# Kernel tuning notes

Measured on AMD Instinct MI355X. Metric: run time of the kernel, lower is better.

## Reference

```python
import jax, jax.numpy as jnp
import numpy as np

EPS = 1e-5


def _conv1x1(x, w, b):
    # x: (B,C,H,W), w: (O,C), b: (O,)
    return jnp.einsum('oc,bchw->bohw', w, x) + b[None, :, None, None]


def _attn(q, k, v):
    # q,k: (B,Dq,H,W); v: (B,C,H,W). Full NxN attention, softmax over keys.
    B, _, H, W = q.shape
    N = H * W
    Q = q.reshape(B, -1, N)
    K = k.reshape(B, -1, N)
    V = v.reshape(B, -1, N)
    A = jax.nn.softmax(jnp.einsum('bci,bcj->bij', Q, K), axis=-1)  # (B,N,N)
    out = jnp.einsum('bcj,bij->bci', V, A)  # out[b,c,i] = sum_j V[b,c,j] A[b,i,j]
    return out.reshape(B, -1, H, W)


def _std(feat):
    # torch.var(dim=2) is unbiased (ddof=1)
    B, C = feat.shape[:2]
    v = jnp.var(feat.reshape(B, C, -1), axis=2, ddof=1) + EPS
    return jnp.sqrt(v)[:, :, None, None]


def _fmm(fb_feat, bg_feat):
    return fb_feat * (_std(bg_feat) / _std(fb_feat))


def setup_inputs() -> dict:
    key = jax.random.key(0)
    ks = jax.random.split(key, 16)
    B, C, H, W = 2, 256, 64, 64
    D = C // 8
    s = 0.05
    inp = {
        'x': jax.random.normal(ks[0], (B, C, H, W), jnp.float32),
        'mask': jax.random.randint(ks[1], (B, 1, H, W), 0, 2).astype(jnp.float32),
        'sa_wq': jax.random.normal(ks[2], (D, C), jnp.float32) * s,
        'sa_bq': jax.random.normal(ks[3], (D,), jnp.float32) * s,
        'sa_wk': jax.random.normal(ks[4], (D, C), jnp.float32) * s,
        'sa_bk': jax.random.normal(ks[5], (D,), jnp.float32) * s,
        'sa_wv': jax.random.normal(ks[6], (C, C), jnp.float32) * s,
        'sa_bv': jax.random.normal(ks[7], (C,), jnp.float32) * s,
        'sa_gamma': jax.random.uniform(ks[8], (1,), jnp.float32),
        'wq': jax.random.normal(ks[9], (D, C), jnp.float32) * s,
        'bq': jax.random.normal(ks[10], (D,), jnp.float32) * s,
        'wk': jax.random.normal(ks[11], (D, C), jnp.float32) * s,
        'bk': jax.random.normal(ks[12], (D,), jnp.float32) * s,
        'wv': jax.random.normal(ks[13], (C, C), jnp.float32) * s,
        'bv': jax.random.normal(ks[14], (C,), jnp.float32) * s,
        'gamma': jax.random.uniform(ks[15], (1,), jnp.float32),
    }
    return inp


def reference(x, mask, sa_wq, sa_bq, sa_wk, sa_bk, sa_wv, sa_bv, sa_gamma,
              wq, bq, wk, bk, wv, bv, gamma):
    # --- Self_Attn ---
    sa_out = _attn(_conv1x1(x, sa_wq, sa_bq),
                   _conv1x1(x, sa_wk, sa_bk),
                   _conv1x1(x, sa_wv, sa_bv))
    x = sa_gamma[0] * sa_out + x
    # --- FB_FMM masked cross attention (mask already at feature resolution) ---
    reverse_mask = 1.0 - mask
    feature_b = reverse_mask * x
    feature_f = mask * x
    sw_bg = _attn(_conv1x1(feature_f, wq, bq),
                  _conv1x1(feature_b, wk, bk),
                  _conv1x1(feature_b, wv, bv))
    out = x + gamma[0] * _fmm(feature_f, sw_bg)
    return out
```

## Files before the change

kernel.cpp:

```cpp
#include <hip/hip_runtime.h>
#include <stdint.h>

typedef _Float16 f16;
typedef __attribute__((ext_vector_type(8))) _Float16 half8;
typedef __attribute__((ext_vector_type(2))) __fp16 fp16x2;
typedef __attribute__((ext_vector_type(8))) short short8;
typedef __attribute__((ext_vector_type(4))) float f32x4;

#define NPOS 4096
#define CCH  256
#define OQK  64
#define BATCH 2
#define NSPLIT 4
#define KEYS_PER_SPLIT 1024

typedef __attribute__((address_space(3))) uint32_t lds_u32;
typedef __attribute__((address_space(1))) const uint32_t glb_u32;

__device__ __forceinline__ float bf2f(short u) {
    union { uint32_t i; float f; } c;
    c.i = ((uint32_t)(uint16_t)u) << 16;
    return c.f;
}
__device__ __forceinline__ short f2bf(float f) {
    union { float f; uint32_t i; } c; c.f = f;
    uint32_t lsb = (c.i >> 16) & 1u;
    c.i += 0x7FFFu + lsb;
    return (short)(c.i >> 16);
}

__device__ __forceinline__ bool detect_bf16(const uint32_t* mw) {
    int hits = 0;
    #pragma unroll
    for (int i = 0; i < 64; ++i) hits += ((mw[i] & 0xFFFFu) == 0x3F80u) ? 1 : 0;
    return hits != 0;
}

__device__ __forceinline__ void load8(const void* base, size_t e0, bool bf, float* v) {
    if (bf) {
        short8 s = *(const short8*)((const short*)base + e0);
        #pragma unroll
        for (int j = 0; j < 8; ++j) v[j] = bf2f(s[j]);
    } else {
        const float* fp = (const float*)base + e0;
        float4 a = *(const float4*)fp;
        float4 b = *(const float4*)(fp + 4);
        v[0] = a.x; v[1] = a.y; v[2] = a.z; v[3] = a.w;
        v[4] = b.x; v[5] = b.y; v[6] = b.z; v[7] = b.w;
    }
}
__device__ __forceinline__ float load1(const void* base, int i, bool bf) {
    return bf ? bf2f(((const short*)base)[i]) : ((const float*)base)[i];
}

__device__ __forceinline__ int pkrtz(float a, float b) {
    union { fp16x2 h; int i; } u;
    u.h = __builtin_amdgcn_cvt_pkrtz(a, b);
    return u.i;
}

__global__ __launch_bounds__(256) void convert_inputs(
    const uint32_t* __restrict__ mask_raw,
    const void* __restrict__ w1q, const void* __restrict__ w1k, const void* __restrict__ w1v_,
    const void* __restrict__ b1q, const void* __restrict__ b1k, const void* __restrict__ b1v_,
    const void* __restrict__ g1,
    const void* __restrict__ w2q, const void* __restrict__ w2k, const void* __restrict__ w2v_,
    const void* __restrict__ b2q, const void* __restrict__ b2k, const void* __restrict__ b2v_,
    const void* __restrict__ g2,
    float* __restrict__ maskf,
    f16* __restrict__ w1qk, f16* __restrict__ w1vm, f16* __restrict__ b1,
    f16* __restrict__ w2qk, f16* __restrict__ w2vm, f16* __restrict__ b2,
    float* __restrict__ gam)
{
    const bool bf = detect_bf16(mask_raw);
    const int blk = blockIdx.x, tid = threadIdx.x;
    float v[8];
    if (blk < 4) {
        const size_t e0 = ((size_t)blk * 256 + tid) * 8;
        load8(mask_raw, e0, bf, v);
        float4 f0 = {v[0], v[1], v[2], v[3]}, f1 = {v[4], v[5], v[6], v[7]};
        *(float4*)(maskf + e0) = f0;
        *(float4*)(maskf + e0 + 4) = f1;
    } else if (blk < 12) {
        const size_t g = ((size_t)(blk - 4) * 256 + tid) * 8;
        const int o = (int)(g >> 8), cc = (int)(g & 255);
        const void* src = (o < 32) ? w1q : w1k;
        const size_t se = (size_t)((o < 32) ? o : o - 32) * 256 + cc;
        load8(src, se, bf, v);
        half8 h;
        #pragma unroll
        for (int j = 0; j < 8; ++j) h[j] = (f16)v[j];
        *(half8*)(w1qk + g) = h;
    } else if (blk < 44) {
        const size_t g = ((size_t)(blk - 12) * 256 + tid) * 8;
        load8(w1v_, g, bf, v);
        half8 h;
        #pragma unroll
        for (int j = 0; j < 8; ++j) h[j] = (f16)v[j];
        *(half8*)(w1vm + g) = h;
    } else if (blk < 52) {
        const size_t g = ((size_t)(blk - 44) * 256 + tid) * 8;
        const int o = (int)(g >> 8), cc = (int)(g & 255);
        const void* src = (o < 32) ? w2q : w2k;
        const size_t se = (size_t)((o < 32) ? o : o - 32) * 256 + cc;
        load8(src, se, bf, v);
        half8 h;
        #pragma unroll
        for (int j = 0; j < 8; ++j) h[j] = (f16)v[j];
        *(half8*)(w2qk + g) = h;
    } else if (blk < 84) {
        const size_t g = ((size_t)(blk - 52) * 256 + tid) * 8;
        load8(w2v_, g, bf, v);
        half8 h;
        #pragma unroll
        for (int j = 0; j < 8; ++j) h[j] = (f16)v[j];
        *(half8*)(w2vm + g) = h;
    } else {
        for (int i = tid; i < 320; i += 256) {
            const void* s1 = (i < 32) ? b1q : (i < 64) ? b1k : b1v_;
            const void* s2 = (i < 32) ? b2q : (i < 64) ? b2k : b2v_;
            const int ii = (i < 32) ? i : (i < 64) ? i - 32 : i - 64;
            b1[i] = (f16)load1(s1, ii, bf);
            b2[i] = (f16)load1(s2, ii, bf);
        }
        if (tid == 0) {
            gam[0] = load1(g1, 0, bf);
            gam[1] = load1(g2, 0, bf);
        }
    }
}

__global__ __launch_bounds__(256) void conv_qkv(
    const void* __restrict__ xin, int is_raw,
    const uint32_t* __restrict__ mask_raw,
    const f16* __restrict__ wqk,
    const f16* __restrict__ wvm,
    const f16* __restrict__ bias,
    const float* __restrict__ maskf, int use_mask,
    f16* __restrict__ qkout,
    f16* __restrict__ vout)
{
    const bool bf = is_raw ? detect_bf16(mask_raw) : false;
    const int b    = blockIdx.y;
    const int n0   = blockIdx.x * 32;
    const int tid  = threadIdx.x;
    const int lane = tid & 63;
    const int w    = tid >> 6;
    const int lo   = lane & 15;
    const int hi   = lane >> 4;

    __shared__ f16 xt[32 * 256];

    {
        const int nc = tid & 3;
        const int cg = tid >> 2;
        #pragma unroll
        for (int it = 0; it < 4; ++it) {
            const int c = cg + 64 * it;
            const size_t off = ((size_t)b * CCH + c) * NPOS + n0 + nc * 8;
            float v8[8];
            load8(xin, off, bf, v8);
            #pragma unroll
            for (int j = 0; j < 8; ++j) {
                const int n = nc * 8 + j;
                int byte = n * 512 + c * 2;
                byte ^= ((n & 7) << 4);
                *(f16*)((char*)xt + byte) = (f16)v8[j];
            }
        }
    }
    __syncthreads();

    const f32x4 z = {0.f, 0.f, 0.f, 0.f};
    f32x4 acc_qk[2];
    f32x4 acc_v[4][2];
    #pragma unroll
    for (int i = 0; i < 2; ++i) {
        acc_qk[i] = z;
        #pragma unroll
        for (int j = 0; j < 4; ++j) acc_v[j][i] = z;
    }

    #pragma unroll 1
    for (int ks = 0; ks < 8; ++ks) {
        const int ce = ks * 32 + 8 * hi;
        half8 xfr[2];
        #pragma unroll
        for (int nt = 0; nt < 2; ++nt) {
            const int n = nt * 16 + lo;
            int byte = n * 512 + ce * 2;
            byte ^= ((n & 7) << 4);
            xfr[nt] = *(const half8*)((const char*)xt + byte);
        }
        {
            half8 wf = *(const half8*)(wqk + (size_t)(w * 16 + lo) * 256 + ce);
            #pragma unroll
            for (int nt = 0; nt < 2; ++nt)
                acc_qk[nt] = __builtin_amdgcn_mfma_f32_16x16x32_f16(xfr[nt], wf, acc_qk[nt], 0, 0, 0);
        }
        #pragma unroll
        for (int ot = 0; ot < 4; ++ot) {
            half8 wf = *(const half8*)(wvm + (size_t)(w * 64 + ot * 16 + lo) * 256 + ce);
            #pragma unroll
            for (int nt = 0; nt < 2; ++nt)
                acc_v[ot][nt] = __builtin_amdgcn_mfma_f32_16x16x32_f16(wf, xfr[nt], acc_v[ot][nt], 0, 0, 0);
        }
    }

    {
        const int o = w * 16 + lo;
        const float bb = (float)bias[o];
        #pragma unroll
        for (int nt = 0; nt < 2; ++nt) {
            #pragma unroll
            for (int r = 0; r < 4; ++r) {
                const int n = n0 + nt * 16 + 4 * hi + r;
                float mult = 1.f;
                if (use_mask) {
                    const float mv = maskf[b * NPOS + n];
                    mult = (o < 32) ? mv : (1.f - mv);
                }
                qkout[((size_t)b * NPOS + n) * OQK + o] = (f16)(mult * acc_qk[nt][r] + bb);
            }
        }
    }
    {
        float mv_n[2];
        #pragma unroll
        for (int nt = 0; nt < 2; ++nt)
            mv_n[nt] = use_mask ? (1.f - maskf[b * NPOS + n0 + nt * 16 + lo]) : 1.f;
        #pragma unroll
        for (int ot = 0; ot < 4; ++ot) {
            #pragma unroll
            for (int r = 0; r < 4; ++r) {
                const int oc = w * 64 + ot * 16 + 4 * hi + r;
                const float bb = (float)bias[64 + oc];
                #pragma unroll
                for (int nt = 0; nt < 2; ++nt) {
                    const int n = n0 + nt * 16 + lo;
                    vout[((size_t)b * CCH + oc) * NPOS + n] = (f16)(mv_n[nt] * acc_v[ot][nt][r] + bb);
                }
            }
        }
    }
}

__global__ __launch_bounds__(256, 2) void attn_split(
    const f16* __restrict__ qk,
    const f16* __restrict__ vbuf,
    f16* __restrict__ po,
    float2* __restrict__ pml)
{
    const int b     = blockIdx.z;
    const int split = blockIdx.y;
    const int tid   = threadIdx.x;
    const int lane  = tid & 63;
    const int w     = tid >> 6;
    const int lo    = lane & 15;
    const int hi    = lane >> 4;
    const int q0    = blockIdx.x * 64;
    const int qown  = w * 16;
    const int qA    = (w >> 1) * 32;
    const int qB    = qA + 16;
    const int cbase = (w & 1) * 128;

    __shared__ f16 kv[(CCH + 64) * 64];
    __shared__ f16 plds[64 * 72];
    __shared__ float sc_lds[64];
    __shared__ float l_lds[64];
    __shared__ int   flag_lds[4];

    const int trow = tid >> 3;
    const int tch  = tid & 7;

    const half8 qfrag = *(const half8*)(qk + ((size_t)b * NPOS + q0 + qown + lo) * OQK + 8 * hi);

    const f32x4 z = {0.f, 0.f, 0.f, 0.f};
    f32x4 accA[8], accB[8];
    #pragma unroll
    for (int i = 0; i < 8; ++i) { accA[i] = z; accB[i] = z; }
    float m_run = -3.0e38f, l_run = 0.f;

    const f16* vsrc = vbuf + (size_t)b * CCH * NPOS;
    const f16* ksrc = qk + (size_t)b * NPOS * OQK;

    #define STAGE(kt)                                                          \
    {                                                                          \
        const int j0s = split * KEYS_PER_SPLIT + (kt) * 64;                    \
        _Pragma("unroll")                                                      \
        for (int i = 0; i < 8; ++i) {                                          \
            const int c = i * 32 + trow;                                       \
            const f16* g = vsrc + (size_t)c * NPOS + j0s + ((tch ^ (c & 7)) * 8); \
            char* d = (char*)kv + i * 4096 + w * 1024;                         \
            __builtin_amdgcn_global_load_lds((glb_u32*)g, (lds_u32*)d, 16, 0, 0); \
        }                                                                      \
        _Pragma("unroll")                                                      \
        for (int i = 0; i < 2; ++i) {                                          \
            const int j = i * 32 + trow;                                       \
            const f16* g = ksrc + (size_t)(j0s + j) * OQK + ((tch ^ (j & 7)) * 8); \
            char* d = (char*)kv + 32768 + i * 4096 + w * 1024;                 \
            __builtin_amdgcn_global_load_lds((glb_u32*)g, (lds_u32*)d, 16, 0, 0); \
        }                                                                      \
    }

    STAGE(0)

    #pragma unroll 1
    for (int kt = 0; kt < KEYS_PER_SPLIT / 64; ++kt) {
        asm volatile("s_waitcnt vmcnt(0)" ::: "memory");
        __syncthreads();

        f32x4 s[4];
        __builtin_amdgcn_s_setprio(1);
        #pragma unroll
        for (int jt = 0; jt < 4; ++jt) {
            const int krow = jt * 16 + lo;
            const half8 kfrag = *(const half8*)((const char*)kv + (CCH + krow) * 128
                                                + ((64 + hi * 16) ^ ((krow & 7) << 4)));
            s[jt] = __builtin_amdgcn_mfma_f32_16x16x32_f16(kfrag, qfrag, z, 0, 0, 0);
        }
        __builtin_amdgcn_s_setprio(0);
        float pm = s[0][0];
        #pragma unroll
        for (int jt = 0; jt < 4; ++jt)
            #pragma unroll
            for (int r = 0; r < 4; ++r) pm = fmaxf(pm, s[jt][r]);
        pm = fmaxf(pm, __shfl_xor(pm, 16, 64));
        pm = fmaxf(pm, __shfl_xor(pm, 32, 64));
        const bool g = __any(pm - m_run > 8.f);
        float scv = 1.f;
        if (g) {
            const float mnew = fmaxf(m_run, pm);
            scv = __expf(m_run - mnew);
            m_run = mnew;
            l_run *= scv;
        }
        float rs = 0.f;
        #pragma unroll
        for (int jt = 0; jt < 4; ++jt) {
            #pragma unroll
            for (int r = 0; r < 4; ++r) {
                const float pv = __expf(s[jt][r] - m_run);
                s[jt][r] = pv;
                rs += pv;
            }
        }
        rs += __shfl_xor(rs, 16, 64);
        rs += __shfl_xor(rs, 32, 64);
        l_run += rs;
        #pragma unroll
        for (int jt = 0; jt < 4; ++jt) {
            union { int i2[2]; uint64_t u; } pw;
            pw.i2[0] = pkrtz(s[jt][0], s[jt][1]);
            pw.i2[1] = pkrtz(s[jt][2], s[jt][3]);
            *(uint64_t*)((char*)plds + (qown + lo) * 144 + jt * 32 + 8 * hi) = pw.u;
        }
        if (hi == 0) sc_lds[qown + lo] = scv;
        if (lane == 0) flag_lds[w] = g ? 1 : 0;
        __syncthreads();

        const int fA = flag_lds[(w >> 1) * 2];
        const int fB = flag_lds[(w >> 1) * 2 + 1];
        if (fA) {
            const float sa = sc_lds[qA + lo];
            #pragma unroll
            for (int ct = 0; ct < 8; ++ct) accA[ct] *= sa;
        }
        if (fB) {
            const float sb = sc_lds[qB + lo];
            #pragma unroll
            for (int ct = 0; ct < 8; ++ct) accB[ct] *= sb;
        }
        __builtin_amdgcn_s_setprio(1);
        #pragma unroll
        for (int ksp = 0; ksp < 2; ++ksp) {
            const half8 pfA = *(const half8*)((const char*)plds + (qA + lo) * 144 + ksp * 64 + 16 * hi);
            const half8 pfB = *(const half8*)((const char*)plds + (qB + lo) * 144 + ksp * 64 + 16 * hi);
            #pragma unroll
            for (int ct = 0; ct < 8; ++ct) {
                const int vrow = cbase + ct * 16 + lo;
                const half8 vfrag = *(const half8*)((const char*)kv + vrow * 128
                                                    + ((ksp * 64 + hi * 16) ^ ((vrow & 7) << 4)));
                accA[ct] = __builtin_amdgcn_mfma_f32_16x16x32_f16(vfrag, pfA, accA[ct], 0, 0, 0);
                accB[ct] = __builtin_amdgcn_mfma_f32_16x16x32_f16(vfrag, pfB, accB[ct], 0, 0, 0);
            }
        }
        __builtin_amdgcn_s_setprio(0);
        __syncthreads();
        if (kt + 1 < KEYS_PER_SPLIT / 64) STAGE(kt + 1)
    }
    #undef STAGE

    if (hi == 0) {
        l_lds[qown + lo] = l_run;
        float2 v; v.x = m_run; v.y = l_run;
        pml[((size_t)split * BATCH + b) * NPOS + q0 + qown + lo] = v;
    }
    __syncthreads();
    const float invA = 1.f / l_lds[qA + lo];
    const float invB = 1.f / l_lds[qB + lo];
    f16* pob = po + (((size_t)split * BATCH + b) * CCH + cbase) * NPOS + q0;
    #pragma unroll
    for (int ct = 0; ct < 8; ++ct) {
        #pragma unroll
        for (int r = 0; r < 4; ++r) {
            const size_t rowo = (size_t)(ct * 16 + 4 * hi + r) * NPOS;
            pob[rowo + qA + lo] = (f16)(accA[ct][r] * invA);
            pob[rowo + qB + lo] = (f16)(accB[ct][r] * invB);
        }
    }
}

__global__ __launch_bounds__(256) void attn_merge(
    const f16* __restrict__ po,
    const float2* __restrict__ pml,
    const void* __restrict__ xraw,
    const uint32_t* __restrict__ mask_raw,
    const float* __restrict__ gamp,
    float* __restrict__ out_f,
    f16* __restrict__ out_h,
    int add_residual)
{
    const int b  = blockIdx.z;
    const int n0 = blockIdx.x * 64;
    const int c0 = blockIdx.y * 32;
    const int tid = threadIdx.x;
    const int cl  = tid >> 3;
    const int oct = tid & 7;

    __shared__ float wls[NSPLIT][64];
    if (tid < 64) {
        const int n = n0 + tid;
        float m[NSPLIT], l[NSPLIT];
        #pragma unroll
        for (int s = 0; s < NSPLIT; ++s) {
            float2 v = pml[((size_t)s * BATCH + b) * NPOS + n];
            m[s] = v.x; l[s] = v.y;
        }
        float M = m[0];
        #pragma unroll
        for (int s = 1; s < NSPLIT; ++s) M = fmaxf(M, m[s]);
        float wgt[NSPLIT], wsum = 0.f;
        #pragma unroll
        for (int s = 0; s < NSPLIT; ++s) { wgt[s] = __expf(m[s] - M) * l[s]; wsum += wgt[s]; }
        const float winv = 1.f / wsum;
        #pragma unroll
        for (int s = 0; s < NSPLIT; ++s) wls[s][tid] = wgt[s] * winv;
    }
    __syncthreads();

    const int c = c0 + cl;
    const int nl = oct * 8;
    const size_t base = ((size_t)b * CCH + c) * NPOS + n0 + nl;
    float o[8] = {0.f, 0.f, 0.f, 0.f, 0.f, 0.f, 0.f, 0.f};
    #pragma unroll
    for (int s = 0; s < NSPLIT; ++s) {
        const half8 pv = *(const half8*)(po + (((size_t)s * BATCH + b) * CCH + c) * NPOS + n0 + nl);
        const float* wr = &wls[s][nl];
        #pragma unroll
        for (int j = 0; j < 8; ++j) o[j] += wr[j] * (float)pv[j];
    }
    if (add_residual) {
        const bool bf = detect_bf16(mask_raw);
        const float gamma = gamp[0];
        float xv[8];
        load8(xraw, base, bf, xv);
        float4 f0, f1;
        f0.x = gamma * o[0] + xv[0]; f0.y = gamma * o[1] + xv[1];
        f0.z = gamma * o[2] + xv[2]; f0.w = gamma * o[3] + xv[3];
        f1.x = gamma * o[4] + xv[4]; f1.y = gamma * o[5] + xv[5];
        f1.z = gamma * o[6] + xv[6]; f1.w = gamma * o[7] + xv[7];
        *(float4*)(out_f + base) = f0;
        *(float4*)(out_f + base + 4) = f1;
    } else {
        half8 h;
        #pragma unroll
        for (int j = 0; j < 8; ++j) h[j] = (f16)o[j];
        *(half8*)(out_h + base) = h;
    }
}

__global__ __launch_bounds__(256) void fmm_final(
    const float* __restrict__ x1f,
    const f16*  __restrict__ bg,
    const float* __restrict__ maskf,
    const float* __restrict__ gamp,
    const uint32_t* __restrict__ mask_raw,
    void* __restrict__ outp)
{
    const bool bf = detect_bf16(mask_raw);
    const int b = blockIdx.y;
    const int c = blockIdx.x;
    const int tid = threadIdx.x;
    const size_t rowoff = ((size_t)b * CCH + c) * NPOS;
    const float* xrow = x1f + rowoff;
    const f16*  grow = bg + rowoff;
    const float* mrow = maskf + (size_t)b * NPOS;

    float s_f = 0.f, ss_f = 0.f, s_g = 0.f, ss_g = 0.f;
    #pragma unroll
    for (int u = 0; u < 2; ++u) {
        const int i = tid * 16 + u * 8;
        const float4 x0 = *(const float4*)(xrow + i);
        const float4 x1v = *(const float4*)(xrow + i + 4);
        const float4 m0 = *(const float4*)(mrow + i);
        const float4 m1 = *(const float4*)(mrow + i + 4);
        half8 gv = *(const half8*)(grow + i);
        const float xs[8] = {x0.x, x0.y, x0.z, x0.w, x1v.x, x1v.y, x1v.z, x1v.w};
        const float ms[8] = {m0.x, m0.y, m0.z, m0.w, m1.x, m1.y, m1.z, m1.w};
        #pragma unroll
        for (int j = 0; j < 8; ++j) {
            const float f = xs[j] * ms[j];
            const float g = (float)gv[j];
            s_f += f; ss_f += f * f;
            s_g += g; ss_g += g * g;
        }
    }
    #pragma unroll
    for (int off = 1; off < 64; off <<= 1) {
        s_f += __shfl_xor(s_f, off, 64);
        ss_f += __shfl_xor(ss_f, off, 64);
        s_g += __shfl_xor(s_g, off, 64);
        ss_g += __shfl_xor(ss_g, off, 64);
    }
    __shared__ float red[4][4];
    const int wv_ = tid >> 6;
    if ((tid & 63) == 0) {
        red[wv_][0] = s_f; red[wv_][1] = ss_f; red[wv_][2] = s_g; red[wv_][3] = ss_g;
    }
    __syncthreads();
    s_f  = red[0][0] + red[1][0] + red[2][0] + red[3][0];
    ss_f = red[0][1] + red[1][1] + red[2][1] + red[3][1];
    s_g  = red[0][2] + red[1][2] + red[2][2] + red[3][2];
    ss_g = red[0][3] + red[1][3] + red[2][3] + red[3][3];

    const float nn = 4096.f, nm1 = 4095.f;
    const float var_f = (ss_f - s_f * s_f / nn) / nm1;
    const float var_g = (ss_g - s_g * s_g / nn) / nm1;
    const float ratio = sqrtf((var_g + 1e-5f) / (var_f + 1e-5f));
    const float gamma = gamp[0];

    #pragma unroll
    for (int u = 0; u < 2; ++u) {
        const int i = tid * 16 + u * 8;
        const float4 x0 = *(const float4*)(xrow + i);
        const float4 x1v = *(const float4*)(xrow + i + 4);
        const float4 m0 = *(const float4*)(mrow + i);
        const float4 m1 = *(const float4*)(mrow + i + 4);
        const float xs[8] = {x0.x, x0.y, x0.z, x0.w, x1v.x, x1v.y, x1v.z, x1v.w};
        const float ms[8] = {m0.x, m0.y, m0.z, m0.w, m1.x, m1.y, m1.z, m1.w};
        float ov[8];
        #pragma unroll
        for (int j = 0; j < 8; ++j)
            ov[j] = xs[j] + gamma * (xs[j] * ms[j]) * ratio;
        if (bf) {
            short8 sv;
            #pragma unroll
            for (int j = 0; j < 8; ++j) sv[j] = f2bf(ov[j]);
            *(short8*)((short*)outp + rowoff + i) = sv;
        } else {
            float4 f0 = {ov[0], ov[1], ov[2], ov[3]}, f1 = {ov[4], ov[5], ov[6], ov[7]};
            *(float4*)((float*)outp + rowoff + i) = f0;
            *(float4*)((float*)outp + rowoff + i + 4) = f1;
        }
    }
}

extern "C" void kernel_launch(void* const* d_in, const int* in_sizes, int n_in,
                              void* d_out, int out_size, void* d_ws, size_t ws_size,
                              hipStream_t stream)
{
    const size_t MB = 1u << 20, KB = 1u << 10;
    char* ws = (char*)d_ws;
    f16*    qkbuf = (f16*)(ws);
    f16*    vbuf  = (f16*)(ws + 1 * MB);
    f16*    bgbuf = (f16*)(ws);
    float*  x1f   = (float*)(ws + 5 * MB);
    f16*    po    = (f16*)(ws + 13 * MB);
    float2* pml   = (float2*)(ws + 29 * MB);
    float*  maskf = (float*)(ws + 29 * MB + 512 * KB);
    f16*    w1qk  = (f16*)(ws + 30 * MB);
    f16*    w1v   = (f16*)(ws + 30 * MB + 32 * KB);
    f16*    b1    = (f16*)(ws + 30 * MB + 160 * KB);
    f16*    w2qk  = (f16*)(ws + 30 * MB + 164 * KB);
    f16*    w2v   = (f16*)(ws + 30 * MB + 196 * KB);
    f16*    b2    = (f16*)(ws + 30 * MB + 324 * KB);
    float*  gam   = (float*)(ws + 30 * MB + 328 * KB);

    const uint32_t* mraw = (const uint32_t*)d_in[1];

    dim3 blk(256);
    dim3 vgrid(85);
    dim3 cgrid(NPOS / 32, BATCH);
    dim3 agrid(NPOS / 64, NSPLIT, BATCH);
    dim3 mgrid(NPOS / 64, CCH / 32, BATCH);
    dim3 fgrid(CCH, BATCH);

    convert_inputs<<<vgrid, blk, 0, stream>>>(
        mraw,
        d_in[2], d_in[4], d_in[6], d_in[3], d_in[5], d_in[7], d_in[8],
        d_in[9], d_in[11], d_in[13], d_in[10], d_in[12], d_in[14], d_in[15],
        maskf, w1qk, w1v, b1, w2qk, w2v, b2, gam);

    conv_qkv<<<cgrid, blk, 0, stream>>>(d_in[0], 1, mraw, w1qk, w1v, b1, maskf, 0, qkbuf, vbuf);
    attn_split<<<agrid, blk, 0, stream>>>(qkbuf, vbuf, po, pml);
    attn_merge<<<mgrid, blk, 0, stream>>>(po, pml, d_in[0], mraw, gam + 0, x1f, nullptr, 1);
    conv_qkv<<<cgrid, blk, 0, stream>>>(x1f, 0, mraw, w2qk, w2v, b2, maskf, 1, qkbuf, vbuf);
    attn_split<<<agrid, blk, 0, stream>>>(qkbuf, vbuf, po, pml);
    attn_merge<<<mgrid, blk, 0, stream>>>(po, pml, nullptr, mraw, gam + 1, nullptr, bgbuf, 0);
    fmm_final<<<fgrid, blk, 0, stream>>>(x1f, bgbuf, maskf, gam + 1, mraw, d_out);
}
```

Before: 125.0 us.

## Double-buffer K tiles and split K/V staging to overlap loads with compute

Moves the key tile into its own double-buffered LDS region and prefetches the next key tile at the start of each iteration, while V is still loaded after the PV step. Waits are relaxed to partial vmcnt counts so QK^T and softmax can proceed while V is still in flight. This aims to hide global-to-LDS load latency behind the score computation, at the cost of extra LDS and counting-based waits that must match the per-thread load order exactly.

```diff
diff --git a/kernel.cpp b/kernel.cpp
--- a/kernel.cpp
+++ b/kernel.cpp
@@ -13,6 +13,7 @@
 #define BATCH 2
 #define NSPLIT 4
 #define KEYS_PER_SPLIT 1024
+#define NT (KEYS_PER_SPLIT / 64)
 
 typedef __attribute__((address_space(3))) uint32_t lds_u32;
 typedef __attribute__((address_space(1))) const uint32_t glb_u32;
@@ -264,7 +265,8 @@
     const int qB    = qA + 16;
     const int cbase = (w & 1) * 128;
 
-    __shared__ f16 kv[(CCH + 64) * 64];
+    __shared__ f16 kv[CCH * 64];
+    __shared__ f16 kbuf[2][64 * 64];
     __shared__ f16 plds[64 * 72];
     __shared__ float sc_lds[64];
     __shared__ float l_lds[64];
@@ -284,7 +286,19 @@
     const f16* vsrc = vbuf + (size_t)b * CCH * NPOS;
     const f16* ksrc = qk + (size_t)b * NPOS * OQK;
 
-    #define STAGE(kt)                                                          \
+    #define STAGE_K(kt)                                                        \
+    {                                                                          \
+        const int j0s = split * KEYS_PER_SPLIT + (kt) * 64;                    \
+        char* kb = (char*)kbuf + ((kt) & 1) * 8192;                            \
+        _Pragma("unroll")                                                      \
+        for (int i = 0; i < 2; ++i) {                                          \
+            const int j = i * 32 + trow;                                       \
+            const f16* g = ksrc + (size_t)(j0s + j) * OQK + ((tch ^ (j & 7)) * 8); \
+            char* d = kb + i * 4096 + w * 1024;                                \
+            __builtin_amdgcn_global_load_lds((glb_u32*)g, (lds_u32*)d, 16, 0, 0); \
+        }                                                                      \
+    }
+    #define STAGE_V(kt)                                                        \
     {                                                                          \
         const int j0s = split * KEYS_PER_SPLIT + (kt) * 64;                    \
         _Pragma("unroll")                                                      \
@@ -294,28 +308,24 @@
             char* d = (char*)kv + i * 4096 + w * 1024;                         \
             __builtin_amdgcn_global_load_lds((glb_u32*)g, (lds_u32*)d, 16, 0, 0); \
         }                                                                      \
-        _Pragma("unroll")                                                      \
-        for (int i = 0; i < 2; ++i) {                                          \
-            const int j = i * 32 + trow;                                       \
-            const f16* g = ksrc + (size_t)(j0s + j) * OQK + ((tch ^ (j & 7)) * 8); \
-            char* d = (char*)kv + 32768 + i * 4096 + w * 1024;                 \
-            __builtin_amdgcn_global_load_lds((glb_u32*)g, (lds_u32*)d, 16, 0, 0); \
-        }                                                                      \
-    }
-
-    STAGE(0)
+    }
+
+    STAGE_K(0)
+    STAGE_V(0)
 
     #pragma unroll 1
-    for (int kt = 0; kt < KEYS_PER_SPLIT / 64; ++kt) {
-        asm volatile("s_waitcnt vmcnt(0)" ::: "memory");
+    for (int kt = 0; kt < NT; ++kt) {
+        asm volatile("s_waitcnt vmcnt(8)" ::: "memory");
         __syncthreads();
-
+        if (kt + 1 < NT) STAGE_K(kt + 1)
+
+        const char* kb = (const char*)kbuf + (kt & 1) * 8192;
         f32x4 s[4];
         __builtin_amdgcn_s_setprio(1);
         #pragma unroll
         for (int jt = 0; jt < 4; ++jt) {
             const int krow = jt * 16 + lo;
-            const half8 kfrag = *(const half8*)((const char*)kv + (CCH + krow) * 128
+            const half8 kfrag = *(const half8*)(kb + krow * 128
                                                 + ((64 + hi * 16) ^ ((krow & 7) << 4)));
             s[jt] = __builtin_amdgcn_mfma_f32_16x16x32_f16(kfrag, qfrag, z, 0, 0, 0);
         }
@@ -357,6 +367,12 @@
         }
         if (hi == 0) sc_lds[qown + lo] = scv;
         if (lane == 0) flag_lds[w] = g ? 1 : 0;
+
+        if (kt + 1 < NT) {
+            asm volatile("s_waitcnt vmcnt(2)" ::: "memory");
+        } else {
+            asm volatile("s_waitcnt vmcnt(0)" ::: "memory");
+        }
         __syncthreads();
 
         const int fA = flag_lds[(w >> 1) * 2];
@@ -387,9 +403,10 @@
         }
         __builtin_amdgcn_s_setprio(0);
         __syncthreads();
-        if (kt + 1 < KEYS_PER_SPLIT / 64) STAGE(kt + 1)
-    }
-    #undef STAGE
+        if (kt + 1 < NT) STAGE_V(kt + 1)
+    }
+    #undef STAGE_K
+    #undef STAGE_V
 
     if (hi == 0) {
         l_lds[qown + lo] = l_run;
```

Result: no change. 125.2 us (+0.2%).
